# Kernel optimization log

Measured on AMD Instinct MI355X. Metric: run time of the kernel, lower is better.

## Reference

```python
import jax, jax.numpy as jnp
import numpy as np

N_NODES = 100000
N_EDGES = 1000000
D_IN = 128
D_HID = 128
D_OUT = 1


def setup_inputs() -> dict:
    key = jax.random.key(0)
    k1, k2, k3, k4, k5, k6, k7 = jax.random.split(key, 7)
    left = jax.random.normal(k1, (N_NODES, D_IN), dtype=jnp.float32)
    right = jax.random.normal(k2, (N_NODES, D_IN), dtype=jnp.float32)
    pairs = jax.random.randint(k3, (2, N_EDGES), 0, N_NODES, dtype=jnp.int64 if jax.config.jax_enable_x64 else jnp.int32)
    # Kaiming-uniform-ish init like torch Linear defaults
    lim1 = 1.0 / np.sqrt(D_IN)
    W1 = jax.random.uniform(k4, (D_IN, D_HID), minval=-lim1, maxval=lim1, dtype=jnp.float32)
    b1 = jax.random.uniform(k5, (D_HID,), minval=-lim1, maxval=lim1, dtype=jnp.float32)
    lim2 = 1.0 / np.sqrt(D_HID)
    W2 = jax.random.uniform(k6, (D_HID, D_OUT), minval=-lim2, maxval=lim2, dtype=jnp.float32)
    b2 = jax.random.uniform(k7, (D_OUT,), minval=-lim2, maxval=lim2, dtype=jnp.float32)
    return {"left": left, "right": right, "pairs": pairs,
            "W1": W1, "b1": b1, "W2": W2, "b2": b2}


def reference(left, right, pairs, W1, b1, W2, b2):
    # Gather endpoint embeddings and elementwise-multiply: [E, D_IN]
    x = left[pairs[0]] * right[pairs[1]]
    # 2-layer MLP (dropout is identity in eval mode): Linear -> ReLU -> Linear
    h = jax.nn.relu(x @ W1 + b1)          # [E, D_HID]
    logits = h @ W2 + b2                   # [E, 1]
    return jax.nn.sigmoid(logits)
```

## Files before the change

### kernel.cpp

```cpp
#include <hip/hip_runtime.h>
#include <hip/hip_bf16.h>

typedef short bf16x8 __attribute__((ext_vector_type(8)));
typedef short short8 __attribute__((ext_vector_type(8)));
typedef float f32x4  __attribute__((ext_vector_type(4)));

#define D     128
#define CH    16
#define WAVES 8
#define BLK   (WAVES*64)

__device__ __forceinline__ short f2bf(float f) {
    unsigned u = __float_as_uint(f);
    u = (u + 0x7fffu + ((u >> 16) & 1u)) >> 16;
    return (short)u;
}
__device__ __forceinline__ float bf2f(short s) {
    return __uint_as_float(((unsigned)(unsigned short)s) << 16);
}

__device__ __forceinline__ int swz(int row, int intra) {
    return (row << 8) + (intra ^ ((row & 7) << 4));
}

__global__ void prep_w1(const float* __restrict__ W1, short* __restrict__ ws) {
    const int idx = blockIdx.x * 256 + threadIdx.x;
    const int k = idx >> 7, c = idx & 127;
    ws[((c << 8) + ((2 * k) ^ ((c & 7) << 4))) >> 1] = f2bf(W1[idx]);
}

__global__ void conv_bf16(const float* __restrict__ src, short* __restrict__ dst,
                          int n8) {
    int i = blockIdx.x * blockDim.x + threadIdx.x;
    const int stride = gridDim.x * blockDim.x;
    for (; i < n8; i += stride) {
        const f32x4 a = ((const f32x4*)src)[2 * i];
        const f32x4 b = ((const f32x4*)src)[2 * i + 1];
        short8 o;
        o[0] = f2bf(a[0]); o[1] = f2bf(a[1]); o[2] = f2bf(a[2]); o[3] = f2bf(a[3]);
        o[4] = f2bf(b[0]); o[5] = f2bf(b[1]); o[6] = f2bf(b[2]); o[7] = f2bf(b[3]);
        ((short8*)dst)[i] = o;
    }
}

template <int MODE>
__global__ __launch_bounds__(BLK, 4)
void edge_decoder_kernel(const float* __restrict__ left,
                         const float* __restrict__ right,
                         const short* __restrict__ leftb,
                         const short* __restrict__ rightb,
                         const int* __restrict__ pairs,
                         const short* __restrict__ w1ws,
                         const float* __restrict__ b1,
                         const float* __restrict__ W2,
                         const float* __restrict__ b2,
                         float* __restrict__ out, int E)
{
    __shared__ char smem[65536];
    char* const w1t = smem;
    char* const xls = smem + 32768 + (threadIdx.x >> 6) * 4096;

    const int tid  = threadIdx.x;
    const int lane = tid & 63;
    const int wid  = tid >> 6;
    const int lg   = lane >> 4;
    const int lm   = lane & 15;
    const int half = lane >> 5;
    const int l32  = lane & 31;

    for (int j = tid; j < 2048; j += BLK)
        *(f32x4*)(w1t + j * 16) = ((const f32x4*)w1ws)[j];

    float b1v[8], w2v[8];
    #pragma unroll
    for (int ct = 0; ct < 8; ++ct) {
        b1v[ct] = b1[ct * 16 + lm];
        w2v[ct] = W2[ct * 16 + lm];
    }
    const float b2s = b2[0];

    __syncthreads();

    const int chunks = (E + CH - 1) / CH;
    const int stride = gridDim.x * WAVES;

    int c = blockIdx.x * WAVES + wid;
    if (c >= chunks) return;

    auto load_idx = [&](int cc) {
        int e0 = cc * CH + lm;
        if (e0 >= E) e0 = E - 1;
        return pairs[half * E + e0];
    };

    int idxv = load_idx(c);

    while (true) {
        const int cn = c + stride;
        const int base = c * CH;
        const int idxv_n = (cn < chunks) ? load_idx(cn) : 0;

        if (MODE == 1) {
            const int q  = lane >> 4;
            const int lq = lane & 15;
            short8 lv[4], rv[4];
            #pragma unroll
            for (int j = 0; j < 4; ++j) {
                const int iL = __shfl(idxv, 4 * j + q);
                lv[j] = *(const short8*)(leftb + iL * D + lq * 8);
            }
            #pragma unroll
            for (int j = 0; j < 4; ++j) {
                const int iR = __shfl(idxv, 32 + 4 * j + q);
                rv[j] = *(const short8*)(rightb + iR * D + lq * 8);
            }
            #pragma unroll
            for (int j = 0; j < 4; ++j) {
                short8 xb;
                #pragma unroll
                for (int e = 0; e < 8; ++e)
                    xb[e] = f2bf(bf2f(lv[j][e]) * bf2f(rv[j][e]));
                *(short8*)(xls + swz(4 * j + q, lq * 16)) = xb;
            }
        } else {
            float4 lv[8], rv[8];
            #pragma unroll
            for (int j = 0; j < 8; ++j) {
                const int eoff = 2 * j + half;
                const int iL = __shfl(idxv, eoff);
                const int iR = __shfl(idxv, 32 + eoff);
                lv[j] = *(const float4*)(left  + iL * D + l32 * 4);
                rv[j] = *(const float4*)(right + iR * D + l32 * 4);
            }
            #pragma unroll
            for (int j = 0; j < 8; ++j) {
                const int eoff = 2 * j + half;
                short4 xb;
                xb.x = f2bf(lv[j].x * rv[j].x);
                xb.y = f2bf(lv[j].y * rv[j].y);
                xb.z = f2bf(lv[j].z * rv[j].z);
                xb.w = f2bf(lv[j].w * rv[j].w);
                *(short4*)(xls + swz(eoff, l32 * 8)) = xb;
            }
        }

        bf16x8 afr[4];
        #pragma unroll
        for (int kt = 0; kt < 4; ++kt)
            afr[kt] = *(const bf16x8*)(xls + swz(lm, kt * 64 + lg * 16));

        f32x4 acc[8];
        #pragma unroll
        for (int ct = 0; ct < 8; ++ct) acc[ct] = (f32x4){0.f, 0.f, 0.f, 0.f};

        #pragma unroll
        for (int kt = 0; kt < 4; ++kt)
            #pragma unroll
            for (int ct = 0; ct < 8; ++ct) {
                const bf16x8 bfr = *(const bf16x8*)(
                    w1t + swz(ct * 16 + lm, kt * 64 + lg * 16));
                acc[ct] = __builtin_amdgcn_mfma_f32_16x16x32_bf16(
                    afr[kt], bfr, acc[ct], 0, 0, 0);
            }

        float p0 = 0.f, p1 = 0.f, p2 = 0.f, p3 = 0.f;
        #pragma unroll
        for (int ct = 0; ct < 8; ++ct) {
            float h0 = fmaxf(acc[ct][0] + b1v[ct], 0.f);
            float h1 = fmaxf(acc[ct][1] + b1v[ct], 0.f);
            float h2 = fmaxf(acc[ct][2] + b1v[ct], 0.f);
            float h3 = fmaxf(acc[ct][3] + b1v[ct], 0.f);
            p0 = fmaf(h0, w2v[ct], p0);
            p1 = fmaf(h1, w2v[ct], p1);
            p2 = fmaf(h2, w2v[ct], p2);
            p3 = fmaf(h3, w2v[ct], p3);
        }
        #pragma unroll
        for (int s = 1; s < 16; s <<= 1) {
            p0 += __shfl_xor(p0, s);
            p1 += __shfl_xor(p1, s);
            p2 += __shfl_xor(p2, s);
            p3 += __shfl_xor(p3, s);
        }
        if (lm < 4) {
            const float pv = (lm & 2) ? ((lm & 1) ? p3 : p2)
                                      : ((lm & 1) ? p1 : p0);
            const int e = base + lg * 4 + lm;
            if (e < E) out[e] = 1.f / (1.f + __expf(-(pv + b2s)));
        }

        if (cn >= chunks) break;
        c = cn;
        idxv = idxv_n;
    }
}

extern "C" void kernel_launch(void* const* d_in, const int* in_sizes, int n_in,
                              void* d_out, int out_size, void* d_ws, size_t ws_size,
                              hipStream_t stream) {
    const float* left  = (const float*)d_in[0];
    const float* right = (const float*)d_in[1];
    const int*   pairs = (const int*)d_in[2];
    const float* W1    = (const float*)d_in[3];
    const float* b1    = (const float*)d_in[4];
    const float* W2    = (const float*)d_in[5];
    const float* b2    = (const float*)d_in[6];
    float* out = (float*)d_out;

    const int E = in_sizes[2] / 2;
    const int chunks = (E + CH - 1) / CH;
    int blocks = 512;
    const int need = (chunks + WAVES - 1) / WAVES;
    if (need < blocks) blocks = need;

    short* const wsp   = (short*)d_ws;
    short* const leftb = wsp + 16384;
    short* const rightb = leftb + in_sizes[0];

    const size_t need_ws = 32768 + (size_t)(in_sizes[0] + in_sizes[1]) * 2;

    prep_w1<<<64, 256, 0, stream>>>(W1, wsp);

    if (ws_size >= need_ws) {
        conv_bf16<<<2048, 256, 0, stream>>>(left,  leftb,  in_sizes[0] / 8);
        conv_bf16<<<2048, 256, 0, stream>>>(right, rightb, in_sizes[1] / 8);
        edge_decoder_kernel<1><<<blocks, BLK, 0, stream>>>(
            left, right, leftb, rightb, pairs, wsp, b1, W2, b2, out, E);
    } else {
        edge_decoder_kernel<0><<<blocks, BLK, 0, stream>>>(
            left, right, leftb, rightb, pairs, wsp, b1, W2, b2, out, E);
    }
}
```

Measured before the change: 107.0 us.

## Bucket-sort edges by source node to improve gather locality

Adds a histogram, scan and scatter pass that groups edges into buckets by left node index, then has the decoder walk contiguous sorted chunks per block and write outputs by original edge id. This is meant to turn left-embedding gathers into mostly cache-resident accesses. It also merges the two bf16 conversion launches into one kernel. The cost is extra launches, an atomic-based scatter, a larger workspace requirement, and 16-byte records read per edge instead of two indices.

Result: slower. 141.7 us (+32.4%).

```diff
diff --git a/kernel.cpp b/kernel.cpp
--- a/kernel.cpp
+++ b/kernel.cpp
@@ -9,6 +9,9 @@
 #define CH    16
 #define WAVES 8
 #define BLK   (WAVES*64)
+#define NB    2048
+#define SBLK  512
+#define STHR  256
 
 __device__ __forceinline__ short f2bf(float f) {
     unsigned u = __float_as_uint(f);
@@ -29,17 +32,79 @@
     ws[((c << 8) + ((2 * k) ^ ((c & 7) << 4))) >> 1] = f2bf(W1[idx]);
 }
 
-__global__ void conv_bf16(const float* __restrict__ src, short* __restrict__ dst,
-                          int n8) {
+__global__ void conv_both(const float* __restrict__ l, const float* __restrict__ r,
+                          short* __restrict__ lb, short* __restrict__ rb,
+                          int n8l, int n8r) {
     int i = blockIdx.x * blockDim.x + threadIdx.x;
-    const int stride = gridDim.x * blockDim.x;
-    for (; i < n8; i += stride) {
-        const f32x4 a = ((const f32x4*)src)[2 * i];
-        const f32x4 b = ((const f32x4*)src)[2 * i + 1];
+    const int st = gridDim.x * blockDim.x;
+    for (; i < n8l + n8r; i += st) {
+        const float* s; short* d; int j;
+        if (i < n8l) { s = l; d = lb; j = i; }
+        else         { s = r; d = rb; j = i - n8l; }
+        const f32x4 a = ((const f32x4*)s)[2 * j];
+        const f32x4 b = ((const f32x4*)s)[2 * j + 1];
         short8 o;
-        o[0] = f2bf(a[0]); o[1] = f2bf(a[1]); o[2] = f2bf(a[2]); o[3] = f2bf(a[3]);
-        o[4] = f2bf(b[0]); o[5] = f2bf(b[1]); o[6] = f2bf(b[2]); o[7] = f2bf(b[3]);
-        ((short8*)dst)[i] = o;
+        o[0]=f2bf(a[0]); o[1]=f2bf(a[1]); o[2]=f2bf(a[2]); o[3]=f2bf(a[3]);
+        o[4]=f2bf(b[0]); o[5]=f2bf(b[1]); o[6]=f2bf(b[2]); o[7]=f2bf(b[3]);
+        ((short8*)d)[i < n8l ? j : j] = o;
+    }
+}
+
+__global__ __launch_bounds__(STHR)
+void edge_histo(const int* __restrict__ pairs, int E, float scale,
+                int* __restrict__ counts, int* __restrict__ bases) {
+    __shared__ int h[NB];
+    for (int b = threadIdx.x; b < NB; b += STHR) h[b] = 0;
+    __syncthreads();
+    const int epb = (E + SBLK - 1) / SBLK;
+    const int lo = blockIdx.x * epb, hi = min(lo + epb, E);
+    for (int e = lo + threadIdx.x; e < hi; e += STHR) {
+        const int bkt = min(NB - 1, (int)((float)pairs[e] * scale));
+        atomicAdd(&h[bkt], 1);
+    }
+    __syncthreads();
+    for (int b = threadIdx.x; b < NB; b += STHR) {
+        const int v = h[b];
+        if (v) bases[blockIdx.x * NB + b] = atomicAdd(&counts[b], v);
+    }
+}
+
+__global__ __launch_bounds__(1024)
+void bucket_scan(int* __restrict__ counts) {
+    __shared__ int a[1024], b[1024];
+    const int t = threadIdx.x;
+    const int c0 = counts[2 * t], c1 = counts[2 * t + 1];
+    a[t] = c0 + c1;
+    __syncthreads();
+    int* src = a; int* dst = b;
+    for (int off = 1; off < 1024; off <<= 1) {
+        int v = src[t];
+        if (t >= off) v += src[t - off];
+        __syncthreads();
+        dst[t] = v;
+        __syncthreads();
+        int* tmp = src; src = dst; dst = tmp;
+    }
+    const int excl = src[t] - (c0 + c1);
+    counts[2 * t]     = excl;
+    counts[2 * t + 1] = excl + c0;
+}
+
+__global__ __launch_bounds__(STHR)
+void edge_scatter(const int* __restrict__ pairs, int E, float scale,
+                  const int* __restrict__ starts, const int* __restrict__ bases,
+                  int4* __restrict__ recs) {
+    __shared__ int rk[NB];
+    for (int b = threadIdx.x; b < NB; b += STHR) rk[b] = 0;
+    __syncthreads();
+    const int epb = (E + SBLK - 1) / SBLK;
+    const int lo = blockIdx.x * epb, hi = min(lo + epb, E);
+    for (int e = lo + threadIdx.x; e < hi; e += STHR) {
+        const int i0 = pairs[e], i1 = pairs[E + e];
+        const int bkt = min(NB - 1, (int)((float)i0 * scale));
+        const int r = atomicAdd(&rk[bkt], 1);
+        const int slot = starts[bkt] + bases[blockIdx.x * NB + bkt] + r;
+        recs[slot] = make_int4(i0, i1, e, 0);
     }
 }
 
@@ -50,6 +115,7 @@
                          const short* __restrict__ leftb,
                          const short* __restrict__ rightb,
                          const int* __restrict__ pairs,
+                         const int4* __restrict__ recs,
                          const short* __restrict__ w1ws,
                          const float* __restrict__ b1,
                          const float* __restrict__ W2,
@@ -78,40 +144,61 @@
         w2v[ct] = W2[ct * 16 + lm];
     }
     const float b2s = b2[0];
-
     __syncthreads();
 
     const int chunks = (E + CH - 1) / CH;
-    const int stride = gridDim.x * WAVES;
-
-    int c = blockIdx.x * WAVES + wid;
-    if (c >= chunks) return;
-
-    auto load_idx = [&](int cc) {
+
+    int c, hiC, stepC;
+    if (MODE == 2) {
+        const int cpb = (chunks + gridDim.x - 1) / gridDim.x;
+        c = blockIdx.x * cpb + wid;
+        hiC = min(blockIdx.x * cpb + cpb, chunks);
+        stepC = WAVES;
+    } else {
+        c = blockIdx.x * WAVES + wid;
+        hiC = chunks;
+        stepC = gridDim.x * WAVES;
+    }
+    if (c >= hiC) return;
+
+    auto ld_sorted = [&](int cc, int& i0v, int& i1v, int& eidv) {
+        const int slot = cc * CH + lm;
+        if (slot < E) {
+            const int4 r = recs[slot];
+            i0v = r.x; i1v = r.y; eidv = r.z;
+        } else { i0v = 0; i1v = 0; eidv = -1; }
+    };
+    auto ld_plain = [&](int cc, int& i0v, int& i1v, int& eidv) {
         int e0 = cc * CH + lm;
+        eidv = (e0 < E) ? e0 : -1;
         if (e0 >= E) e0 = E - 1;
-        return pairs[half * E + e0];
+        i0v = pairs[e0]; i1v = pairs[E + e0];
     };
 
-    int idxv = load_idx(c);
+    int i0v, i1v, eidv;
+    if (MODE == 2) ld_sorted(c, i0v, i1v, eidv); else ld_plain(c, i0v, i1v, eidv);
 
     while (true) {
-        const int cn = c + stride;
-        const int base = c * CH;
-        const int idxv_n = (cn < chunks) ? load_idx(cn) : 0;
-
-        if (MODE == 1) {
+        const int cn = c + stepC;
+        const bool has = cn < hiC;
+        int i0n = 0, i1n = 0, eidn = -1;
+        if (has) {
+            if (MODE == 2) ld_sorted(cn, i0n, i1n, eidn);
+            else           ld_plain(cn, i0n, i1n, eidn);
+        }
+
+        if (MODE >= 1) {
             const int q  = lane >> 4;
             const int lq = lane & 15;
             short8 lv[4], rv[4];
             #pragma unroll
             for (int j = 0; j < 4; ++j) {
-                const int iL = __shfl(idxv, 4 * j + q);
+                const int iL = __shfl(i0v, 4 * j + q);
                 lv[j] = *(const short8*)(leftb + iL * D + lq * 8);
             }
             #pragma unroll
             for (int j = 0; j < 4; ++j) {
-                const int iR = __shfl(idxv, 32 + 4 * j + q);
+                const int iR = __shfl(i1v, 4 * j + q);
                 rv[j] = *(const short8*)(rightb + iR * D + lq * 8);
             }
             #pragma unroll
@@ -127,8 +214,8 @@
             #pragma unroll
             for (int j = 0; j < 8; ++j) {
                 const int eoff = 2 * j + half;
-                const int iL = __shfl(idxv, eoff);
-                const int iR = __shfl(idxv, 32 + eoff);
+                const int iL = __shfl(i0v, eoff);
+                const int iR = __shfl(i1v, eoff);
                 lv[j] = *(const float4*)(left  + iL * D + l32 * 4);
                 rv[j] = *(const float4*)(right + iR * D + l32 * 4);
             }
@@ -182,16 +269,15 @@
             p2 += __shfl_xor(p2, s);
             p3 += __shfl_xor(p3, s);
         }
-        if (lm < 4) {
+        const int myeid = __shfl(eidv, (lg * 4 + lm) & 15);
+        if (lm < 4 && myeid >= 0) {
             const float pv = (lm & 2) ? ((lm & 1) ? p3 : p2)
                                       : ((lm & 1) ? p1 : p0);
-            const int e = base + lg * 4 + lm;
-            if (e < E) out[e] = 1.f / (1.f + __expf(-(pv + b2s)));
-        }
-
-        if (cn >= chunks) break;
-        c = cn;
-        idxv = idxv_n;
+            out[myeid] = 1.f / (1.f + __expf(-(pv + b2s)));
+        }
+
+        if (!has) break;
+        c = cn; i0v = i0n; i1v = i1n; eidv = eidn;
     }
 }
 
@@ -207,27 +293,54 @@
     const float* b2    = (const float*)d_in[6];
     float* out = (float*)d_out;
 
-    const int E = in_sizes[2] / 2;
+    const int E  = in_sizes[2] / 2;
+    const int nn = in_sizes[0] / D;
     const int chunks = (E + CH - 1) / CH;
-    int blocks = 512;
-    const int need = (chunks + WAVES - 1) / WAVES;
-    if (need < blocks) blocks = need;
-
-    short* const wsp   = (short*)d_ws;
-    short* const leftb = wsp + 16384;
-    short* const rightb = leftb + in_sizes[0];
-
-    const size_t need_ws = 32768 + (size_t)(in_sizes[0] + in_sizes[1]) * 2;
-
-    prep_w1<<<64, 256, 0, stream>>>(W1, wsp);
-
-    if (ws_size >= need_ws) {
-        conv_bf16<<<2048, 256, 0, stream>>>(left,  leftb,  in_sizes[0] / 8);
-        conv_bf16<<<2048, 256, 0, stream>>>(right, rightb, in_sizes[1] / 8);
+    const float scale = (float)NB / (float)nn;
+
+    char* const ws = (char*)d_ws;
+    const size_t offL   = 32768;
+    const size_t szL    = (size_t)in_sizes[0] * 2;
+    const size_t offR   = offL + szL;
+    const size_t szR    = (size_t)in_sizes[1] * 2;
+    const size_t offCnt = offR + szR;
+    const size_t offBas = offCnt + (size_t)NB * 4;
+    const size_t offRec = offBas + (size_t)SBLK * NB * 4;
+    const size_t needSort = offRec + (size_t)chunks * CH * 16;
+    const size_t needBf   = offCnt;
+
+    short* const w1img  = (short*)ws;
+    short* const leftb  = (short*)(ws + offL);
+    short* const rightb = (short*)(ws + offR);
+    int*   const counts = (int*)(ws + offCnt);
+    int*   const bases  = (int*)(ws + offBas);
+    int4*  const recs   = (int4*)(ws + offRec);
+
+    prep_w1<<<64, 256, 0, stream>>>(W1, w1img);
+
+    if (ws_size >= needSort) {
+        conv_both<<<2048, 256, 0, stream>>>(left, right, leftb, rightb,
+                                            in_sizes[0] / 8, in_sizes[1] / 8);
+        hipMemsetAsync(counts, 0, NB * 4, stream);
+        edge_histo<<<SBLK, STHR, 0, stream>>>(pairs, E, scale, counts, bases);
+        bucket_scan<<<1, 1024, 0, stream>>>(counts);
+        edge_scatter<<<SBLK, STHR, 0, stream>>>(pairs, E, scale, counts, bases, recs);
+        int blocks = 512;
+        edge_decoder_kernel<2><<<blocks, BLK, 0, stream>>>(
+            left, right, leftb, rightb, pairs, recs, w1img, b1, W2, b2, out, E);
+    } else if (ws_size >= needBf) {
+        conv_both<<<2048, 256, 0, stream>>>(left, right, leftb, rightb,
+                                            in_sizes[0] / 8, in_sizes[1] / 8);
+        int blocks = 512;
+        const int need = (chunks + WAVES - 1) / WAVES;
+        if (need < blocks) blocks = need;
         edge_decoder_kernel<1><<<blocks, BLK, 0, stream>>>(
-            left, right, leftb, rightb, pairs, wsp, b1, W2, b2, out, E);
+            left, right, leftb, rightb, pairs, recs, w1img, b1, W2, b2, out, E);
     } else {
+        int blocks = 512;
+        const int need = (chunks + WAVES - 1) / WAVES;
+        if (need < blocks) blocks = need;
         edge_decoder_kernel<0><<<blocks, BLK, 0, stream>>>(
-            left, right, leftb, rightb, pairs, wsp, b1, W2, b2, out, E);
-    }
-}
+            left, right, leftb, rightb, pairs, recs, w1img, b1, W2, b2, out, E);
+    }
+}
```
